# Optimization experiments

Hardware: AMD Instinct MI355X
Metric: run time of the kernel (lower is better)

## Reference

```python
import jax, jax.numpy as jnp
import numpy as np

B, S, H = 4, 1024, 1024
NH = 16
DH = H // NH  # 64


def setup_inputs() -> dict:
    key = jax.random.key(0)
    ks = jax.random.split(key, 8)
    std = 1.0 / np.sqrt(H)
    return {
        "query": jax.random.normal(ks[0], (B, S, H), jnp.float32),
        "key": jax.random.normal(ks[1], (B, S, H), jnp.float32),
        "value": jax.random.normal(ks[2], (B, S, H), jnp.float32),
        "masks": jnp.ones((B, S), jnp.float32),
        "Wq": jax.random.normal(ks[3], (H, H), jnp.float32) * std,
        "bq": jnp.zeros((H,), jnp.float32),
        "Wk": jax.random.normal(ks[4], (H, H), jnp.float32) * std,
        "bk": jnp.zeros((H,), jnp.float32),
        "Wv": jax.random.normal(ks[5], (H, H), jnp.float32) * std,
        "bv": jnp.zeros((H,), jnp.float32),
    }


def reference(query, key, value, masks, Wq, bq, Wk, bk, Wv, bv):
    # ReLU-gated projections (torch Linear: x @ W.T + b)
    qp = jax.nn.relu(jnp.einsum("bsh,oh->bso", query, Wq) + bq)
    kp = jax.nn.relu(jnp.einsum("bsh,oh->bso", key, Wk) + bk)
    vp = jax.nn.relu(jnp.einsum("bsh,oh->bso", value, Wv) + bv)
    # chunk(dim=2)+cat(dim=0) == split hidden into (NH, DH) contiguous slices
    qh = qp.reshape(B, S, NH, DH)
    kh = kp.reshape(B, S, NH, DH)
    vh = vp.reshape(B, S, NH, DH)
    scale = 1.0 / jnp.sqrt(jnp.asarray(DH, qp.dtype))
    # [B, NH, Sq, Sk]
    alpha = jnp.einsum("bqnd,bknd->bnqk", qh, kh) * scale
    alpha = jax.nn.softmax(alpha, axis=-1)
    # post-softmax multiplicative mask, applied per QUERY position
    alpha = alpha * masks[:, None, :, None]
    hiddens = jnp.einsum("bnqk,bknd->bqnd", alpha, vh).reshape(B, S, H)
    return hiddens + query
```

## Files before the change

### kernel.cpp

```cpp
#include <hip/hip_runtime.h>


typedef __attribute__((ext_vector_type(8))) __bf16 bf16x8;
typedef __attribute__((ext_vector_type(4))) float f32x4;
typedef __attribute__((ext_vector_type(16))) float f32x16;
typedef __attribute__((ext_vector_type(8))) unsigned short u16x8;
typedef __attribute__((ext_vector_type(4))) unsigned short u16x4;

#define XQ_OFF 0u
#define XK_OFF 4194304u
#define XV_OFF 8388608u
#define WQ_OFF 12582912u
#define WK_OFF 13631488u
#define WV_OFF 14680064u
#define QP_OFF 15728640u
#define KP_OFF 19922944u
#define VT_OFF 24117248u

__device__ __forceinline__ unsigned short f2bf(float f) {
  union { float f; unsigned int u; } c; c.f = f;
  return (unsigned short)((c.u + 0x7fffu + ((c.u >> 16) & 1u)) >> 16);
}

__global__ __launch_bounds__(256) void cvt_kernel(
    const float* __restrict__ q, const float* __restrict__ k, const float* __restrict__ v,
    const float* __restrict__ wq, const float* __restrict__ wk, const float* __restrict__ wv,
    unsigned short* __restrict__ ws) {
  const int z = blockIdx.y;
  const float* src; unsigned short* dst; int n;
  switch (z) {
    case 0: src = q;  dst = ws + XQ_OFF; n = 4194304; break;
    case 1: src = k;  dst = ws + XK_OFF; n = 4194304; break;
    case 2: src = v;  dst = ws + XV_OFF; n = 4194304; break;
    case 3: src = wq; dst = ws + WQ_OFF; n = 1048576; break;
    case 4: src = wk; dst = ws + WK_OFF; n = 1048576; break;
    default: src = wv; dst = ws + WV_OFF; n = 1048576; break;
  }
  const int i8 = (blockIdx.x * 256 + threadIdx.x) * 8;
  if (i8 >= n) return;
  const float4 f0 = *(const float4*)(src + i8);
  const float4 f1 = *(const float4*)(src + i8 + 4);
  u16x8 r;
  r[0] = f2bf(f0.x); r[1] = f2bf(f0.y); r[2] = f2bf(f0.z); r[3] = f2bf(f0.w);
  r[4] = f2bf(f1.x); r[5] = f2bf(f1.y); r[6] = f2bf(f1.z); r[7] = f2bf(f1.w);
  *(u16x8*)(dst + i8) = r;
}

__global__ __launch_bounds__(256) void proj_gemm(
    unsigned short* __restrict__ ws,
    const float* __restrict__ bq, const float* __restrict__ bk, const float* __restrict__ bv) {
  __shared__ unsigned short smem[24576];
  const int z = blockIdx.z;
  const unsigned short* X = ws + (z == 0 ? XQ_OFF : z == 1 ? XK_OFF : XV_OFF);
  const unsigned short* W = ws + (z == 0 ? WQ_OFF : z == 1 ? WK_OFF : WV_OFF);
  unsigned short* P = ws + (z == 0 ? QP_OFF : z == 1 ? KP_OFF : VT_OFF);
  const float* bias = z == 0 ? bq : z == 1 ? bk : bv;

  const int tid  = threadIdx.x;
  const int lane = tid & 63;
  const int w    = tid >> 6;
  const int l31  = lane & 31;
  const int g    = lane >> 5;
  const int wr = w >> 1, wc = w & 1;

  const int lin = blockIdx.x + 8 * blockIdx.y;
  const int xcd = lin & 7;
  const int idx = lin >> 3;
  const int m0 = (xcd * 4 + (idx >> 3)) * 128;
  const int n0 = (idx & 7) * 128;

  f32x16 acc[2][2];
#pragma unroll
  for (int i = 0; i < 2; ++i)
#pragma unroll
    for (int j = 0; j < 2; ++j)
#pragma unroll
      for (int r = 0; r < 16; ++r) acc[i][j][r] = 0.f;

  const int c1 = 256 + tid;
  const int row0 = tid >> 2, kc0 = (((tid & 3) ^ ((row0 >> 1) & 3)) * 8);
  const int row1 = c1 >> 2,  kc1 = (((c1 & 3) ^ ((row1 >> 1) & 3)) * 8);
  const unsigned short* gA0 = X + (size_t)(m0 + row0) * 1024 + kc0;
  const unsigned short* gA1 = X + (size_t)(m0 + row1) * 1024 + kc1;
  const unsigned short* gB0 = W + (size_t)(n0 + row0) * 1024 + kc0;
  const unsigned short* gB1 = W + (size_t)(n0 + row1) * 1024 + kc1;
  const int d0 = w * 512, d1 = 2048 + w * 512;

  auto stage = [&](int buf) {
    unsigned short* Ab = smem + buf * 8192;
    unsigned short* Bb = Ab + 4096;
    __builtin_amdgcn_global_load_lds((const __attribute__((address_space(1))) void*)gA0,
                                     (__attribute__((address_space(3))) void*)(Ab + d0), 16, 0, 0);
    __builtin_amdgcn_global_load_lds((const __attribute__((address_space(1))) void*)gB0,
                                     (__attribute__((address_space(3))) void*)(Bb + d0), 16, 0, 0);
    __builtin_amdgcn_global_load_lds((const __attribute__((address_space(1))) void*)gA1,
                                     (__attribute__((address_space(3))) void*)(Ab + d1), 16, 0, 0);
    __builtin_amdgcn_global_load_lds((const __attribute__((address_space(1))) void*)gB1,
                                     (__attribute__((address_space(3))) void*)(Bb + d1), 16, 0, 0);
    gA0 += 32; gA1 += 32; gB0 += 32; gB1 += 32;
  };
  auto compute = [&](int buf) {
    const unsigned short* Ab = smem + buf * 8192;
    const unsigned short* Bb = Ab + 4096;
    bf16x8 af[2][2], bfv[2][2];
#pragma unroll
    for (int mt = 0; mt < 2; ++mt)
#pragma unroll
      for (int kk = 0; kk < 2; ++kk) {
        const int ra = wr * 64 + mt * 32 + l31;
        af[mt][kk] = *(const bf16x8*)&Ab[ra * 32 + (((kk * 2 + g) ^ ((ra >> 1) & 3)) * 8)];
      }
#pragma unroll
    for (int nt = 0; nt < 2; ++nt)
#pragma unroll
      for (int kk = 0; kk < 2; ++kk) {
        const int rb = wc * 64 + nt * 32 + l31;
        bfv[nt][kk] = *(const bf16x8*)&Bb[rb * 32 + (((kk * 2 + g) ^ ((rb >> 1) & 3)) * 8)];
      }
    __builtin_amdgcn_s_setprio(1);
#pragma unroll
    for (int mt = 0; mt < 2; ++mt)
#pragma unroll
      for (int nt = 0; nt < 2; ++nt)
#pragma unroll
        for (int kk = 0; kk < 2; ++kk)
          acc[mt][nt] = __builtin_amdgcn_mfma_f32_32x32x16_bf16(af[mt][kk], bfv[nt][kk],
                                                                acc[mt][nt], 0, 0, 0);
    __builtin_amdgcn_s_setprio(0);
  };

  stage(0); stage(1);
  for (int t = 0; t < 31; ++t) {
    asm volatile("s_waitcnt vmcnt(4)" ::: "memory");
    __builtin_amdgcn_s_barrier();
    if (t < 30) stage((t + 2) % 3);
    compute(t % 3);
  }
  asm volatile("s_waitcnt vmcnt(0)" ::: "memory");
  __builtin_amdgcn_s_barrier();
  compute(31 % 3);

  asm volatile("s_waitcnt lgkmcnt(0)" ::: "memory");
  __builtin_amdgcn_s_barrier();

  unsigned short* Tw = smem + w * 4608;
  if (z != 2) {
#pragma unroll
    for (int mt = 0; mt < 2; ++mt)
#pragma unroll
      for (int nt = 0; nt < 2; ++nt) {
        const float bvv = bias[n0 + wc * 64 + nt * 32 + l31];
#pragma unroll
        for (int reg = 0; reg < 16; ++reg) {
          const int rloc = (reg & 3) + 8 * (reg >> 2) + 4 * g;
          float v = acc[mt][nt][reg] + bvv;
          v = v > 0.f ? v : 0.f;
          Tw[(mt * 32 + rloc) * 72 + nt * 32 + l31] = f2bf(v);
        }
      }
    const int row0g = m0 + wr * 64;
    const int colb  = n0 + wc * 64;
#pragma unroll
    for (int i = 0; i < 8; ++i) {
      const int rr = i * 8 + (lane >> 3);
      const int cc = (lane & 7) * 8;
      *(u16x8*)&P[(size_t)(row0g + rr) * 1024 + colb + cc] = *(const u16x8*)&Tw[rr * 72 + cc];
    }
  } else {
#pragma unroll
    for (int mt = 0; mt < 2; ++mt)
#pragma unroll
      for (int nt = 0; nt < 2; ++nt) {
        const float bvv = bias[n0 + wc * 64 + nt * 32 + l31];
#pragma unroll
        for (int rq = 0; rq < 4; ++rq) {
          u16x4 pk;
#pragma unroll
          for (int r = 0; r < 4; ++r) {
            float v = acc[mt][nt][rq * 4 + r] + bvv;
            v = v > 0.f ? v : 0.f;
            pk[r] = f2bf(v);
          }
          *(u16x4*)&Tw[(nt * 32 + l31) * 72 + mt * 32 + rq * 8 + g * 4] = pk;
        }
      }
    const int h2 = (n0 >> 6) + wc;
    const int bb = m0 >> 10;
    const int s0 = (m0 & 1023) + wr * 64;
#pragma unroll
    for (int i = 0; i < 8; ++i) {
      const int rr = i * 8 + (lane >> 3);
      const int cc = (lane & 7) * 8;
      *(u16x8*)&P[((size_t)(bb * 16 + h2) * 64 + rr) * 1024 + s0 + cc] =
          *(const u16x8*)&Tw[rr * 72 + cc];
    }
  }
}

__global__ __launch_bounds__(256, 2) void attn_kernel(
    const unsigned short* __restrict__ QP, const unsigned short* __restrict__ KP,
    const unsigned short* __restrict__ VT, const float* __restrict__ masks,
    const float* __restrict__ query, float* __restrict__ out) {
  __shared__ unsigned short Kt[3][64 * 64];
  __shared__ unsigned short Vt[3][64 * 64];
  __shared__ unsigned short Pl[4][32 * 72];
  const int tid  = threadIdx.x;
  const int lane = tid & 63;
  const int w    = tid >> 6;
  const int quad = lane >> 4;
  const int l15  = lane & 15;
  const int bh = blockIdx.x;
  const int b = bh >> 4, h = bh & 15;
  const int q0w = blockIdx.y * 128 + w * 32;
  const size_t base = (size_t)b * 1024 * 1024;

  bf16x8 qf[2][2];
#pragma unroll
  for (int mt = 0; mt < 2; ++mt)
#pragma unroll
    for (int kk = 0; kk < 2; ++kk)
      qf[mt][kk] = *(const bf16x8*)&QP[base + (size_t)(q0w + mt * 16 + l15) * 1024 +
                                       h * 64 + kk * 32 + quad * 8];

  f32x4 o[2][4];
  f32x4 lacc[2];
#pragma unroll
  for (int mt = 0; mt < 2; ++mt) {
    lacc[mt] = f32x4{0.f, 0.f, 0.f, 0.f};
#pragma unroll
    for (int nd = 0; nd < 4; ++nd) o[mt][nd] = f32x4{0.f, 0.f, 0.f, 0.f};
  }

  bf16x8 onesb;
#pragma unroll
  for (int i = 0; i < 8; ++i) onesb[i] = (__bf16)1.0f;

  const int r_st = lane >> 3;
  const int pc   = lane & 7;
  const int swz  = l15 & 7;
  const float cvt = 0.18033688011112042f;

  auto stage = [&](int key0, int buf) {
#pragma unroll
    for (int t = 0; t < 2; ++t) {
      const int rowk = (w * 2 + t) * 8 + r_st;
      const int lc   = pc ^ (rowk & 7);
      const unsigned short* gk = &KP[base + (size_t)(key0 + rowk) * 1024 + h * 64 + lc * 8];
      const unsigned short* gv = &VT[((size_t)bh * 64 + rowk) * 1024 + key0 + lc * 8];
      __builtin_amdgcn_global_load_lds((const __attribute__((address_space(1))) void*)gk,
                                       (__attribute__((address_space(3))) void*)&Kt[buf][(w * 2 + t) * 512],
                                       16, 0, 0);
      __builtin_amdgcn_global_load_lds((const __attribute__((address_space(1))) void*)gv,
                                       (__attribute__((address_space(3))) void*)&Vt[buf][(w * 2 + t) * 512],
                                       16, 0, 0);
    }
  };

  auto step = [&](int buf) {
    const unsigned short* Ktb = Kt[buf];
    const unsigned short* Vtb = Vt[buf];

    bf16x8 kf[2][4];
#pragma unroll
    for (int kk = 0; kk < 2; ++kk)
#pragma unroll
      for (int ni = 0; ni < 4; ++ni)
        kf[kk][ni] = *(const bf16x8*)&Ktb[(ni * 16 + l15) * 64 + ((kk * 4 + quad) ^ swz) * 8];

#pragma unroll
    for (int mt = 0; mt < 2; ++mt) {
      f32x4 st[4];
#pragma unroll
      for (int ni = 0; ni < 4; ++ni) st[ni] = f32x4{0.f, 0.f, 0.f, 0.f};
      __builtin_amdgcn_s_setprio(1);
#pragma unroll
      for (int kk = 0; kk < 2; ++kk)
#pragma unroll
        for (int ni = 0; ni < 4; ++ni)
          st[ni] = __builtin_amdgcn_mfma_f32_16x16x32_bf16(kf[kk][ni], qf[mt][kk], st[ni], 0, 0, 0);
      __builtin_amdgcn_s_setprio(0);
#pragma unroll
      for (int ni = 0; ni < 4; ++ni) {
        float p0 = __builtin_amdgcn_exp2f(fmaf(st[ni][0], cvt, -8.0f));
        float p1 = __builtin_amdgcn_exp2f(fmaf(st[ni][1], cvt, -8.0f));
        float p2 = __builtin_amdgcn_exp2f(fmaf(st[ni][2], cvt, -8.0f));
        float p3 = __builtin_amdgcn_exp2f(fmaf(st[ni][3], cvt, -8.0f));
        const unsigned int u0 = __float_as_uint(p0) + 0x8000u;
        const unsigned int u1 = __float_as_uint(p1) + 0x8000u;
        const unsigned int u2 = __float_as_uint(p2) + 0x8000u;
        const unsigned int u3 = __float_as_uint(p3) + 0x8000u;
        uint2 pk;
        pk.x = (u0 >> 16) | (u1 & 0xffff0000u);
        pk.y = (u2 >> 16) | (u3 & 0xffff0000u);
        *(uint2*)&Pl[w][(mt * 16 + l15) * 72 + ni * 16 + quad * 4] = pk;
      }
    }

#pragma unroll
    for (int kk = 0; kk < 2; ++kk) {
      bf16x8 pa[2];
#pragma unroll
      for (int mt = 0; mt < 2; ++mt)
        pa[mt] = *(const bf16x8*)&Pl[w][(mt * 16 + l15) * 72 + kk * 32 + quad * 8];
      __builtin_amdgcn_s_setprio(1);
#pragma unroll
      for (int mt = 0; mt < 2; ++mt)
        lacc[mt] = __builtin_amdgcn_mfma_f32_16x16x32_bf16(pa[mt], onesb, lacc[mt], 0, 0, 0);
#pragma unroll
      for (int nd = 0; nd < 4; ++nd) {
        bf16x8 vf = *(const bf16x8*)&Vtb[(nd * 16 + l15) * 64 + ((kk * 4 + quad) ^ swz) * 8];
#pragma unroll
        for (int mt = 0; mt < 2; ++mt)
          o[mt][nd] = __builtin_amdgcn_mfma_f32_16x16x32_bf16(pa[mt], vf, o[mt][nd], 0, 0, 0);
      }
      __builtin_amdgcn_s_setprio(0);
    }
  };

  stage(0, 0);
  stage(64, 1);
  for (int kb = 0; kb < 15; ++kb) {
    asm volatile("s_waitcnt vmcnt(4)" ::: "memory");
    __builtin_amdgcn_s_barrier();
    if (kb < 14) stage((kb + 2) * 64, (kb + 2) % 3);
    step(kb % 3);
  }
  asm volatile("s_waitcnt vmcnt(0)" ::: "memory");
  __builtin_amdgcn_s_barrier();
  step(0);

#pragma unroll
  for (int mt = 0; mt < 2; ++mt)
#pragma unroll
    for (int r = 0; r < 4; ++r) {
      const int rq = quad * 4 + r;
      const int row = q0w + mt * 16 + rq;
      const float scale = masks[b * 1024 + row] / lacc[mt][r];
#pragma unroll
      for (int nd = 0; nd < 4; ++nd) {
        const int col = h * 64 + nd * 16 + l15;
        const size_t gi = base + (size_t)row * 1024 + col;
        out[gi] = o[mt][nd][r] * scale + query[gi];
      }
    }
}

extern "C" void kernel_launch(void* const* d_in, const int* in_sizes, int n_in,
                              void* d_out, int out_size, void* d_ws, size_t ws_size,
                              hipStream_t stream) {
  const float* q     = (const float*)d_in[0];
  const float* k     = (const float*)d_in[1];
  const float* v     = (const float*)d_in[2];
  const float* masks = (const float*)d_in[3];
  const float* Wq    = (const float*)d_in[4];
  const float* bq    = (const float*)d_in[5];
  const float* Wk    = (const float*)d_in[6];
  const float* bk    = (const float*)d_in[7];
  const float* Wv    = (const float*)d_in[8];
  const float* bv    = (const float*)d_in[9];
  float* out = (float*)d_out;
  unsigned short* ws = (unsigned short*)d_ws;

  cvt_kernel<<<dim3(2048, 6), 256, 0, stream>>>(q, k, v, Wq, Wk, Wv, ws);
  proj_gemm<<<dim3(8, 32, 3), 256, 0, stream>>>(ws, bq, bk, bv);
  attn_kernel<<<dim3(64, 8), 256, 0, stream>>>(ws + QP_OFF, ws + KP_OFF, ws + VT_OFF,
                                               masks, q, out);
}
```

Before: 174.5 us.

## Fuse fp32-to-bf16 activation conversion into projection GEMM A-operand loading

The separate conversion pass over the three fp32 activation tensors is removed. The projection GEMM now loads fp32 activations into registers, converts them to bf16 and writes them to the swizzled LDS tile itself, while weights still go through global_load_lds. This drops a full read and write of the bf16 activation copies, in exchange for register-staged A loads and a manually rotated software pipeline with hand-placed waitcnts. The GEMM also reads twice as many bytes for A as before.

```diff
diff --git a/kernel.cpp b/kernel.cpp
--- a/kernel.cpp
+++ b/kernel.cpp
@@ -22,22 +22,13 @@
   return (unsigned short)((c.u + 0x7fffu + ((c.u >> 16) & 1u)) >> 16);
 }
 
-__global__ __launch_bounds__(256) void cvt_kernel(
-    const float* __restrict__ q, const float* __restrict__ k, const float* __restrict__ v,
+__global__ __launch_bounds__(256) void cvtw_kernel(
     const float* __restrict__ wq, const float* __restrict__ wk, const float* __restrict__ wv,
     unsigned short* __restrict__ ws) {
   const int z = blockIdx.y;
-  const float* src; unsigned short* dst; int n;
-  switch (z) {
-    case 0: src = q;  dst = ws + XQ_OFF; n = 4194304; break;
-    case 1: src = k;  dst = ws + XK_OFF; n = 4194304; break;
-    case 2: src = v;  dst = ws + XV_OFF; n = 4194304; break;
-    case 3: src = wq; dst = ws + WQ_OFF; n = 1048576; break;
-    case 4: src = wk; dst = ws + WK_OFF; n = 1048576; break;
-    default: src = wv; dst = ws + WV_OFF; n = 1048576; break;
-  }
+  const float* src = z == 0 ? wq : z == 1 ? wk : wv;
+  unsigned short* dst = ws + (z == 0 ? WQ_OFF : z == 1 ? WK_OFF : WV_OFF);
   const int i8 = (blockIdx.x * 256 + threadIdx.x) * 8;
-  if (i8 >= n) return;
   const float4 f0 = *(const float4*)(src + i8);
   const float4 f1 = *(const float4*)(src + i8 + 4);
   u16x8 r;
@@ -47,11 +38,12 @@
 }
 
 __global__ __launch_bounds__(256) void proj_gemm(
+    const float* __restrict__ xq, const float* __restrict__ xk, const float* __restrict__ xv,
     unsigned short* __restrict__ ws,
     const float* __restrict__ bq, const float* __restrict__ bk, const float* __restrict__ bv) {
   __shared__ unsigned short smem[24576];
   const int z = blockIdx.z;
-  const unsigned short* X = ws + (z == 0 ? XQ_OFF : z == 1 ? XK_OFF : XV_OFF);
+  const float* XF = z == 0 ? xq : z == 1 ? xk : xv;
   const unsigned short* W = ws + (z == 0 ? WQ_OFF : z == 1 ? WK_OFF : WV_OFF);
   unsigned short* P = ws + (z == 0 ? QP_OFF : z == 1 ? KP_OFF : VT_OFF);
   const float* bias = z == 0 ? bq : z == 1 ? bk : bv;
@@ -80,24 +72,40 @@
   const int c1 = 256 + tid;
   const int row0 = tid >> 2, kc0 = (((tid & 3) ^ ((row0 >> 1) & 3)) * 8);
   const int row1 = c1 >> 2,  kc1 = (((c1 & 3) ^ ((row1 >> 1) & 3)) * 8);
-  const unsigned short* gA0 = X + (size_t)(m0 + row0) * 1024 + kc0;
-  const unsigned short* gA1 = X + (size_t)(m0 + row1) * 1024 + kc1;
+  const float* gAf0 = XF + (size_t)(m0 + row0) * 1024 + kc0;
+  const float* gAf1 = XF + (size_t)(m0 + row1) * 1024 + kc1;
   const unsigned short* gB0 = W + (size_t)(n0 + row0) * 1024 + kc0;
   const unsigned short* gB1 = W + (size_t)(n0 + row1) * 1024 + kc1;
   const int d0 = w * 512, d1 = 2048 + w * 512;
 
-  auto stage = [&](int buf) {
-    unsigned short* Ab = smem + buf * 8192;
-    unsigned short* Bb = Ab + 4096;
-    __builtin_amdgcn_global_load_lds((const __attribute__((address_space(1))) void*)gA0,
-                                     (__attribute__((address_space(3))) void*)(Ab + d0), 16, 0, 0);
+  f32x4 arA[4], arB[4];
+
+  auto aload = [&](f32x4 (&bank)[4]) {
+    bank[0] = *(const f32x4*)gAf0; bank[1] = *(const f32x4*)(gAf0 + 4);
+    bank[2] = *(const f32x4*)gAf1; bank[3] = *(const f32x4*)(gAf1 + 4);
+    gAf0 += 32; gAf1 += 32;
+  };
+  auto issueB = [&](int buf) {
+    unsigned short* Bb = smem + buf * 8192 + 4096;
     __builtin_amdgcn_global_load_lds((const __attribute__((address_space(1))) void*)gB0,
                                      (__attribute__((address_space(3))) void*)(Bb + d0), 16, 0, 0);
-    __builtin_amdgcn_global_load_lds((const __attribute__((address_space(1))) void*)gA1,
-                                     (__attribute__((address_space(3))) void*)(Ab + d1), 16, 0, 0);
     __builtin_amdgcn_global_load_lds((const __attribute__((address_space(1))) void*)gB1,
                                      (__attribute__((address_space(3))) void*)(Bb + d1), 16, 0, 0);
-    gA0 += 32; gA1 += 32; gB0 += 32; gB1 += 32;
+    gB0 += 32; gB1 += 32;
+  };
+  auto awrite = [&](int buf, const f32x4 (&bank)[4]) {
+    unsigned short* Ab = smem + buf * 8192;
+    bf16x8 w0, w1;
+    w0[0] = (__bf16)bank[0][0]; w0[1] = (__bf16)bank[0][1];
+    w0[2] = (__bf16)bank[0][2]; w0[3] = (__bf16)bank[0][3];
+    w0[4] = (__bf16)bank[1][0]; w0[5] = (__bf16)bank[1][1];
+    w0[6] = (__bf16)bank[1][2]; w0[7] = (__bf16)bank[1][3];
+    w1[0] = (__bf16)bank[2][0]; w1[1] = (__bf16)bank[2][1];
+    w1[2] = (__bf16)bank[2][2]; w1[3] = (__bf16)bank[2][3];
+    w1[4] = (__bf16)bank[3][0]; w1[5] = (__bf16)bank[3][1];
+    w1[6] = (__bf16)bank[3][2]; w1[7] = (__bf16)bank[3][3];
+    *(bf16x8*)&Ab[tid * 8] = w0;
+    *(bf16x8*)&Ab[2048 + tid * 8] = w1;
   };
   auto compute = [&](int buf) {
     const unsigned short* Ab = smem + buf * 8192;
@@ -129,16 +137,37 @@
     __builtin_amdgcn_s_setprio(0);
   };
 
-  stage(0); stage(1);
-  for (int t = 0; t < 31; ++t) {
-    asm volatile("s_waitcnt vmcnt(4)" ::: "memory");
+  auto body = [&](int bufC, int bufW, int bufB, const f32x4 (&bw)[4], f32x4 (&bl)[4]) {
+    asm volatile("s_waitcnt vmcnt(2) lgkmcnt(0)" ::: "memory");
     __builtin_amdgcn_s_barrier();
-    if (t < 30) stage((t + 2) % 3);
-    compute(t % 3);
+    awrite(bufW, bw);
+    aload(bl);
+    issueB(bufB);
+    compute(bufC);
+  };
+
+  aload(arA);
+  issueB(0);
+  aload(arB);
+  issueB(1);
+  asm volatile("s_waitcnt vmcnt(8)" ::: "memory");
+  awrite(0, arA);
+
+  for (int it = 0; it < 5; ++it) {
+    body(0, 1, 2, arB, arA);
+    body(1, 2, 0, arA, arB);
+    body(2, 0, 1, arB, arA);
+    body(0, 1, 2, arA, arB);
+    body(1, 2, 0, arB, arA);
+    body(2, 0, 1, arA, arB);
   }
-  asm volatile("s_waitcnt vmcnt(0)" ::: "memory");
+  asm volatile("s_waitcnt vmcnt(2) lgkmcnt(0)" ::: "memory");
   __builtin_amdgcn_s_barrier();
-  compute(31 % 3);
+  awrite(1, arB);
+  compute(0);
+  asm volatile("s_waitcnt vmcnt(0) lgkmcnt(0)" ::: "memory");
+  __builtin_amdgcn_s_barrier();
+  compute(1);
 
   asm volatile("s_waitcnt lgkmcnt(0)" ::: "memory");
   __builtin_amdgcn_s_barrier();
@@ -361,8 +390,8 @@
   float* out = (float*)d_out;
   unsigned short* ws = (unsigned short*)d_ws;
 
-  cvt_kernel<<<dim3(2048, 6), 256, 0, stream>>>(q, k, v, Wq, Wk, Wv, ws);
-  proj_gemm<<<dim3(8, 32, 3), 256, 0, stream>>>(ws, bq, bk, bv);
+  cvtw_kernel<<<dim3(512, 3), 256, 0, stream>>>(Wq, Wk, Wv, ws);
+  proj_gemm<<<dim3(8, 32, 3), 256, 0, stream>>>(q, k, v, ws, bq, bk, bv);
   attn_kernel<<<dim3(64, 8), 256, 0, stream>>>(ws + QP_OFF, ws + KP_OFF, ws + VT_OFF,
                                                masks, q, out);
 }
```

Result: slower. 198.5 us (+13.7%).
